# Kernel tuning notes

Hardware: AMD Instinct MI355X
Metric: run time of the kernel (lower is better)

Reference implementation:

```python
import jax, jax.numpy as jnp
import numpy as np

def setup_inputs() -> dict:
    key = jax.random.key(0)
    k1, k2 = jax.random.split(key)
    B, S, D, R = 16, 1024, 1024, 128
    batch = jax.random.normal(k1, (B, S, D), dtype=jnp.float32)
    # probe parameter initialized uniform(-0.05, 0.05) as in the torch module
    proj = jax.random.uniform(k2, (D, R), dtype=jnp.float32, minval=-0.05, maxval=0.05)
    return {"batch": batch, "proj": proj}

def reference(batch, proj):
    # transformed: [B, S, R]
    t = jnp.matmul(batch, proj)
    # squared L2 distances for all pairs: ||t_i||^2 + ||t_j||^2 - 2 t_i . t_j
    sq_norms = jnp.sum(t * t, axis=-1)                      # [B, S]
    cross = jnp.einsum('bir,bjr->bij', t, t)                # [B, S, S]
    d = sq_norms[:, :, None] + sq_norms[:, None, :] - 2.0 * cross
    return jnp.maximum(d, 0.0)  # clamp tiny negative values from the identity
```

## Files before the change

kernel.cpp:

```cpp
#include <hip/hip_runtime.h>

typedef __attribute__((ext_vector_type(8))) __bf16 bf16x8;
typedef __attribute__((ext_vector_type(4))) __bf16 bf16x4;
typedef __attribute__((ext_vector_type(4))) float f32x4;

#define B_ 16
#define S_ 1024
#define D_ 1024
#define R_ 128

__global__ __launch_bounds__(256) void k_transpose(const float* __restrict__ proj,
                                                   __bf16* __restrict__ projT) {
    __shared__ __bf16 tile[64][66];
    const int k0 = blockIdx.x * 64;
    const int r0 = blockIdx.y * 64;
#pragma unroll
    for (int it = 0; it < 16; ++it) {
        int idx = it * 256 + threadIdx.x;
        int kk = idx >> 6, rr = idx & 63;
        tile[kk][rr] = (__bf16)proj[(size_t)(k0 + kk) * R_ + (r0 + rr)];
    }
    __syncthreads();
#pragma unroll
    for (int it = 0; it < 16; ++it) {
        int idx = it * 256 + threadIdx.x;
        int rr = idx >> 6, kk = idx & 63;
        projT[(size_t)(r0 + rr) * D_ + (k0 + kk)] = tile[kk][rr];
    }
}

#define STG_LD 264
__global__ __launch_bounds__(256, 4) void k_proj(const float* __restrict__ batch,
                                                 const __bf16* __restrict__ projT,
                                                 __bf16* __restrict__ t,
                                                 float* __restrict__ sqn) {
    const int wave = threadIdx.x >> 6;
    const int lane = threadIdx.x & 63;
    const int ln = lane & 15;
    const int q  = lane >> 4;
    const int m0 = blockIdx.x * 16;
    const int kbase = wave * 256;

    __shared__ __align__(16) char smraw[4 * 16 * STG_LD * 2];
    __bf16 (*stg)[STG_LD] =
        reinterpret_cast<__bf16(*)[STG_LD]>(smraw + wave * (16 * STG_LD * 2));

    const float* abase = batch + (size_t)m0 * D_ + kbase;
#pragma unroll
    for (int r = 0; r < 16; ++r) {
        float4 v = *(const float4*)(abase + (size_t)r * D_ + lane * 4);
        bf16x4 h = {(__bf16)v.x, (__bf16)v.y, (__bf16)v.z, (__bf16)v.w};
        *(bf16x4*)&stg[r][lane * 4] = h;
    }

    f32x4 acc[8];
#pragma unroll
    for (int ni = 0; ni < 8; ++ni) acc[ni] = f32x4{0.f, 0.f, 0.f, 0.f};

#pragma unroll
    for (int k0 = 0; k0 < 256; k0 += 32) {
        const int ka = k0 + q * 8;
        bf16x8 af = *(const bf16x8*)&stg[ln][ka];
#pragma unroll
        for (int ni = 0; ni < 8; ++ni) {
            bf16x8 bf = *(const bf16x8*)(projT + (size_t)(ni * 16 + ln) * D_ + kbase + ka);
            acc[ni] = __builtin_amdgcn_mfma_f32_16x16x32_bf16(af, bf, acc[ni], 0, 0, 0);
        }
    }

    __syncthreads();
    f32x4 (*red)[64] = reinterpret_cast<f32x4(*)[64]>(smraw);
    float (*sqpart)[16] = reinterpret_cast<float(*)[16]>(smraw + 32768);
#pragma unroll
    for (int ni = 0; ni < 8; ++ni) red[wave * 8 + ni][lane] = acc[ni];
    __syncthreads();

    float sq[4] = {0.f, 0.f, 0.f, 0.f};
#pragma unroll
    for (int p = 0; p < 2; ++p) {
        const int ni = wave * 2 + p;
        f32x4 v = red[ni][lane];
#pragma unroll
        for (int w = 1; w < 4; ++w) {
            f32x4 u = red[w * 8 + ni][lane];
            v[0] += u[0]; v[1] += u[1]; v[2] += u[2]; v[3] += u[3];
        }
#pragma unroll
        for (int r = 0; r < 4; ++r) {
            __bf16 h = (__bf16)v[r];
            t[(size_t)(m0 + q * 4 + r) * R_ + ni * 16 + ln] = h;
            float f = (float)h;
            sq[r] += f * f;
        }
    }
#pragma unroll
    for (int r = 0; r < 4; ++r) {
#pragma unroll
        for (int off = 1; off < 16; off <<= 1)
            sq[r] += __shfl_xor(sq[r], off, 64);
    }
    if (ln == 0) {
#pragma unroll
        for (int r = 0; r < 4; ++r) sqpart[wave][q * 4 + r] = sq[r];
    }
    __syncthreads();
    if (threadIdx.x < 16) {
        float s = sqpart[0][threadIdx.x] + sqpart[1][threadIdx.x] +
                  sqpart[2][threadIdx.x] + sqpart[3][threadIdx.x];
        sqn[m0 + threadIdx.x] = s;
    }
}

__global__ __launch_bounds__(256, 4) void k_gram(const __bf16* __restrict__ t,
                                                 const float* __restrict__ sqn,
                                                 float* __restrict__ out) {
    const int b = blockIdx.z;
    const int wave = threadIdx.x >> 6;
    const int lane = threadIdx.x & 63;
    const int ln = lane & 15;
    const int q  = lane >> 4;
    const int wi = wave >> 1, wj = wave & 1;
    const int i0 = blockIdx.y * 128 + wi * 64;
    const int j0 = blockIdx.x * 128 + wj * 64;
    const __bf16* tb = t + (size_t)b * S_ * R_;
    const float* sqb = sqn + (size_t)b * S_;

    f32x4 acc[4][4];
#pragma unroll
    for (int mi = 0; mi < 4; ++mi)
#pragma unroll
        for (int ni = 0; ni < 4; ++ni) acc[mi][ni] = f32x4{0.f, 0.f, 0.f, 0.f};

#pragma unroll
    for (int k0 = 0; k0 < R_; k0 += 32) {
        const int ka = k0 + q * 8;
        bf16x8 af[4], bfm[4];
#pragma unroll
        for (int mi = 0; mi < 4; ++mi)
            af[mi] = *(const bf16x8*)(tb + (size_t)(i0 + mi * 16 + ln) * R_ + ka);
#pragma unroll
        for (int ni = 0; ni < 4; ++ni)
            bfm[ni] = *(const bf16x8*)(tb + (size_t)(j0 + ni * 16 + ln) * R_ + ka);
#pragma unroll
        for (int mi = 0; mi < 4; ++mi)
#pragma unroll
            for (int ni = 0; ni < 4; ++ni)
                acc[mi][ni] = __builtin_amdgcn_mfma_f32_16x16x32_bf16(
                    af[mi], bfm[ni], acc[mi][ni], 0, 0, 0);
    }

    float sqj[4];
#pragma unroll
    for (int ni = 0; ni < 4; ++ni) sqj[ni] = sqb[j0 + ni * 16 + ln];

    float* outb = out + (size_t)b * S_ * S_;
#pragma unroll
    for (int mi = 0; mi < 4; ++mi) {
        float4 si4 = *(const float4*)(sqb + i0 + mi * 16 + q * 4);
#pragma unroll
        for (int ni = 0; ni < 4; ++ni) {
            const int j = j0 + ni * 16 + ln;
            float4 o;
            o.x = fmaxf(si4.x + sqj[ni] - 2.f * acc[mi][ni][0], 0.f);
            o.y = fmaxf(si4.y + sqj[ni] - 2.f * acc[mi][ni][1], 0.f);
            o.z = fmaxf(si4.z + sqj[ni] - 2.f * acc[mi][ni][2], 0.f);
            o.w = fmaxf(si4.w + sqj[ni] - 2.f * acc[mi][ni][3], 0.f);
            *(float4*)(outb + (size_t)j * S_ + i0 + mi * 16 + q * 4) = o;
        }
    }
}

extern "C" void kernel_launch(void* const* d_in, const int* in_sizes, int n_in,
                              void* d_out, int out_size, void* d_ws, size_t ws_size,
                              hipStream_t stream) {
    const float* batch = (const float*)d_in[0];
    const float* proj  = (const float*)d_in[1];
    float* out = (float*)d_out;

    char* ws = (char*)d_ws;
    __bf16* t     = (__bf16*)ws;
    __bf16* projT = (__bf16*)(ws + (size_t)B_ * S_ * R_ * 2);
    float*  sqn   = (float*)(ws + (size_t)B_ * S_ * R_ * 2
                                + (size_t)R_ * D_ * 2);

    k_transpose<<<dim3(D_ / 64, R_ / 64), 256, 0, stream>>>(proj, projT);
    k_proj<<<dim3((B_ * S_) / 16), 256, 0, stream>>>(batch, projT, t, sqn);
    k_gram<<<dim3(S_ / 128, S_ / 128, B_), 256, 0, stream>>>(t, sqn, out);
}
```

Before: 157.5 us.

## Stage gram tiles in LDS and software-pipeline projT loads in projection

```diff
diff --git a/kernel.cpp b/kernel.cpp
--- a/kernel.cpp
+++ b/kernel.cpp
@@ -57,14 +57,28 @@
 #pragma unroll
     for (int ni = 0; ni < 8; ++ni) acc[ni] = f32x4{0.f, 0.f, 0.f, 0.f};
 
-#pragma unroll
-    for (int k0 = 0; k0 < 256; k0 += 32) {
-        const int ka = k0 + q * 8;
-        bf16x8 af = *(const bf16x8*)&stg[ln][ka];
-#pragma unroll
-        for (int ni = 0; ni < 8; ++ni) {
-            bf16x8 bf = *(const bf16x8*)(projT + (size_t)(ni * 16 + ln) * D_ + kbase + ka);
-            acc[ni] = __builtin_amdgcn_mfma_f32_16x16x32_bf16(af, bf, acc[ni], 0, 0, 0);
+    const __bf16* bbase = projT + kbase;
+    const int ka0 = q * 8;
+    bf16x8 bcur[8], bnxt[8];
+#pragma unroll
+    for (int ni = 0; ni < 8; ++ni)
+        bcur[ni] = *(const bf16x8*)(bbase + (size_t)(ni * 16 + ln) * D_ + ka0);
+
+#pragma unroll
+    for (int k0 = 0; k0 < 8; ++k0) {
+        if (k0 < 7) {
+            const int kan = ka0 + (k0 + 1) * 32;
+#pragma unroll
+            for (int ni = 0; ni < 8; ++ni)
+                bnxt[ni] = *(const bf16x8*)(bbase + (size_t)(ni * 16 + ln) * D_ + kan);
+        }
+        bf16x8 af = *(const bf16x8*)&stg[ln][k0 * 32 + ka0];
+#pragma unroll
+        for (int ni = 0; ni < 8; ++ni)
+            acc[ni] = __builtin_amdgcn_mfma_f32_16x16x32_bf16(af, bcur[ni], acc[ni], 0, 0, 0);
+        if (k0 < 7) {
+#pragma unroll
+            for (int ni = 0; ni < 8; ++ni) bcur[ni] = bnxt[ni];
         }
     }
 
@@ -111,7 +125,8 @@
     }
 }
 
-__global__ __launch_bounds__(256, 4) void k_gram(const __bf16* __restrict__ t,
+#define GLP 264
+__global__ __launch_bounds__(256, 2) void k_gram(const __bf16* __restrict__ t,
                                                  const float* __restrict__ sqn,
                                                  float* __restrict__ out) {
     const int b = blockIdx.z;
@@ -120,27 +135,45 @@
     const int ln = lane & 15;
     const int q  = lane >> 4;
     const int wi = wave >> 1, wj = wave & 1;
-    const int i0 = blockIdx.y * 128 + wi * 64;
-    const int j0 = blockIdx.x * 128 + wj * 64;
+    const int i0b = blockIdx.y * 128;
+    const int j0b = blockIdx.x * 128;
     const __bf16* tb = t + (size_t)b * S_ * R_;
     const float* sqb = sqn + (size_t)b * S_;
 
+    __shared__ __align__(16) char sm[256 * GLP];
+    {
+        const __bf16* tis = tb + (size_t)i0b * R_;
+        const __bf16* tjs = tb + (size_t)j0b * R_;
+#pragma unroll
+        for (int it = 0; it < 16; ++it) {
+            int u = it * 256 + threadIdx.x;
+            int row = u >> 4, ch = u & 15;
+            const __bf16* src = (row < 128) ? (tis + (size_t)row * R_)
+                                            : (tjs + (size_t)(row - 128) * R_);
+            float4 v = *(const float4*)(src + ch * 8);
+            *(float4*)(sm + (size_t)row * GLP + ch * 16) = v;
+        }
+    }
+    __syncthreads();
+
     f32x4 acc[4][4];
 #pragma unroll
     for (int mi = 0; mi < 4; ++mi)
 #pragma unroll
         for (int ni = 0; ni < 4; ++ni) acc[mi][ni] = f32x4{0.f, 0.f, 0.f, 0.f};
 
+    const char* ibase = sm + (size_t)(wi * 64) * GLP;
+    const char* jbase = sm + (size_t)(128 + wj * 64) * GLP;
 #pragma unroll
     for (int k0 = 0; k0 < R_; k0 += 32) {
-        const int ka = k0 + q * 8;
+        const int kab = (k0 + q * 8) * 2;
         bf16x8 af[4], bfm[4];
 #pragma unroll
         for (int mi = 0; mi < 4; ++mi)
-            af[mi] = *(const bf16x8*)(tb + (size_t)(i0 + mi * 16 + ln) * R_ + ka);
+            af[mi] = *(const bf16x8*)(ibase + (size_t)(mi * 16 + ln) * GLP + kab);
 #pragma unroll
         for (int ni = 0; ni < 4; ++ni)
-            bfm[ni] = *(const bf16x8*)(tb + (size_t)(j0 + ni * 16 + ln) * R_ + ka);
+            bfm[ni] = *(const bf16x8*)(jbase + (size_t)(ni * 16 + ln) * GLP + kab);
 #pragma unroll
         for (int mi = 0; mi < 4; ++mi)
 #pragma unroll
@@ -149,6 +182,8 @@
                     af[mi], bfm[ni], acc[mi][ni], 0, 0, 0);
     }
 
+    const int i0 = i0b + wi * 64;
+    const int j0 = j0b + wj * 64;
     float sqj[4];
 #pragma unroll
     for (int ni = 0; ni < 4; ++ni) sqj[ni] = sqb[j0 + ni * 16 + ln];
```

Result: no change. 159.6 us (+1.3%).
